# Performance work log

Hardware: AMD Instinct MI355X
Metric: run time of the kernel (lower is better)

The kernel has to match this reference:

```python
import jax, jax.numpy as jnp
import numpy as np

HEIGHT, WIDTH = 384, 640


def setup_inputs() -> dict:
    key = jax.random.key(0)
    ks = jax.random.split(key, 6)
    B, N, C_CLS, D = 8, 100, 92, 256
    return {
        "images": jax.random.normal(ks[0], (B, 3, HEIGHT, WIDTH), dtype=jnp.float32),
        "logits": jax.random.normal(ks[1], (B, N, C_CLS), dtype=jnp.float32),
        "pred_boxes": jax.random.uniform(ks[2], (B, N, 4), dtype=jnp.float32),
        "last_hidden_state": jax.random.normal(ks[3], (B, N, D), dtype=jnp.float32),
        "fc_w": jax.random.normal(ks[4], (256, D), dtype=jnp.float32) * 0.05,
        "fc_b": jax.random.normal(ks[5], (256,), dtype=jnp.float32) * 0.05,
    }


def reference(images, logits, pred_boxes, last_hidden_state, fc_w, fc_b):
    B = images.shape[0]
    num_objects = 2

    # probas computed in the original forward (unused in training mode -> DCE'd)
    probas = jax.nn.softmax(logits, axis=-1)[:, :, :-1]

    # cxcywh -> xyxy, scale by [W, H, W, H], truncate to int (torch .int())
    cx, cy, w, h = jnp.split(pred_boxes, 4, axis=-1)  # each [B, N, 1]
    xyxy = jnp.concatenate([cx - 0.5 * w, cy - 0.5 * h, cx + 0.5 * w, cy + 0.5 * h], axis=-1)
    img_dims = jnp.array([WIDTH, HEIGHT, WIDTH, HEIGHT], dtype=jnp.float32)
    bboxes = (xyxy * img_dims).astype(jnp.int32)  # [B, N, 4]

    # bboxes_to_mask (faithful to original, incl. its x/y axis convention):
    # x indexes rows (height), y indexes columns (width)
    x = jnp.arange(HEIGHT, dtype=jnp.float32)[:, None]   # [H, 1]
    y = jnp.arange(WIDTH, dtype=jnp.float32)[None, :]    # [1, W]
    bb = bboxes.astype(jnp.float32)[:, :, :, None, None]  # [B, N, 4, 1, 1]
    masks = (bb[:, :, 0] <= x) & (x <= bb[:, :, 2]) & (bb[:, :, 1] <= y) & (y <= bb[:, :, 3])  # [B, N, H, W]

    # diff images: sum channels, pairwise diff over (pre, post), abs, repeat x2 on batch
    summed = images.sum(axis=1).reshape(B // 2, 2, HEIGHT, WIDTH)
    diff = jnp.abs(summed[:, 1:] - summed[:, :1])          # [B/2, 1, H, W]
    diff = jnp.repeat(diff, 2, axis=0)                     # [B, 1, H, W]

    # masked mean score per box
    scores = jnp.mean(jnp.where(masks, diff, jnp.float32(0.0)), axis=(2, 3))  # [B, N]

    _, indices = jax.lax.top_k(scores, num_objects)        # [B, num_objects]
    h_i = jnp.take_along_axis(last_hidden_state, indices[:, :, None], axis=1)  # [B, O, D]
    h_i = h_i @ fc_w.T + fc_b                              # Linear: x W^T + b
    h_i = h_i.reshape(B // 2, 2, num_objects, -1)          # [b, i=2, O, hidden]
    return h_i[:, 0], h_i[:, 1]
```

## Files before the change

### kernel.cpp

```cpp
#include <hip/hip_runtime.h>

#define H_IMG 384
#define W_IMG 640
#define NPAIR 4
#define NBATCH 8
#define NBOX 100
#define DHID 256
#define ROWTILE 8
#define NTILES (H_IMG / ROWTILE)

__global__ __launch_bounds__(256) void k_sat_tile(const float* __restrict__ images,
                                                  float* __restrict__ sat,
                                                  float* __restrict__ totals_t) {
    __shared__ float buf[ROWTILE][W_IMG];

    const int p    = blockIdx.x / NTILES;
    const int tile = blockIdx.x % NTILES;
    const int lane = threadIdx.x & 63;
    const int wv   = threadIdx.x >> 6;
    const int r_lo = tile * ROWTILE;

    const size_t chw  = (size_t)H_IMG * W_IMG;
    const size_t chw2 = chw / 2;

    for (int rr = wv; rr < ROWTILE; rr += 4) {
        const int h = r_lo + rr;
        const float2* i0 = (const float2*)(images + ((size_t)(2 * p)     * 3 * H_IMG + h) * W_IMG);
        const float2* i1 = (const float2*)(images + ((size_t)(2 * p + 1) * 3 * H_IMG + h) * W_IMG);

        float dxv[5], dyv[5], s[5];
        #pragma unroll
        for (int k = 0; k < 5; ++k) {
            const int e = k * 64 + lane;
            float2 a0 = i0[e], b0 = i0[e + chw2], c0 = i0[e + 2 * chw2];
            float2 a1 = i1[e], b1 = i1[e + chw2], c1 = i1[e + 2 * chw2];
            dxv[k] = fabsf(((a1.x + b1.x) + c1.x) - ((a0.x + b0.x) + c0.x));
            dyv[k] = fabsf(((a1.y + b1.y) + c1.y) - ((a0.y + b0.y) + c0.y));
            s[k]   = dxv[k] + dyv[k];
        }

        #pragma unroll
        for (int off = 1; off < 64; off <<= 1) {
            float u0 = __shfl_up(s[0], off, 64);
            float u1 = __shfl_up(s[1], off, 64);
            float u2 = __shfl_up(s[2], off, 64);
            float u3 = __shfl_up(s[3], off, 64);
            float u4 = __shfl_up(s[4], off, 64);
            if (lane >= off) {
                s[0] += u0; s[1] += u1; s[2] += u2; s[3] += u3; s[4] += u4;
            }
        }

        const float t0 = __shfl(s[0], 63, 64);
        const float t1 = __shfl(s[1], 63, 64);
        const float t2 = __shfl(s[2], 63, 64);
        const float t3 = __shfl(s[3], 63, 64);
        float base[5];
        base[0] = 0.0f;
        base[1] = t0;
        base[2] = t0 + t1;
        base[3] = base[2] + t2;
        base[4] = base[3] + t3;

        float2* brow = (float2*)buf[rr];
        #pragma unroll
        for (int k = 0; k < 5; ++k) {
            const int e = k * 64 + lane;
            const float excl = base[k] + s[k] - (dxv[k] + dyv[k]);
            brow[e] = make_float2(excl + dxv[k], excl + dxv[k] + dyv[k]);
        }
    }
    __syncthreads();

    const int t = threadIdx.x;
    #pragma unroll
    for (int sub = 0; sub < 3; ++sub) {
        const int c = sub * 256 + t;
        if (c < W_IMG) {
            float run = 0.0f;
            float* gcol = sat + ((size_t)p * H_IMG + r_lo) * W_IMG + c;
            #pragma unroll
            for (int i = 0; i < ROWTILE; ++i) {
                run += buf[i][c];
                gcol[(size_t)i * W_IMG] = run;
            }
            totals_t[((size_t)p * W_IMG + c) * NTILES + tile] = run;
        }
    }
}

__global__ __launch_bounds__(256) void k_score_topk_fc(
        const float* __restrict__ sat,
        const float* __restrict__ totals_t,
        const float* __restrict__ pred_boxes,
        const float* __restrict__ lhs,
        const float* __restrict__ fc_w,
        const float* __restrict__ fc_b,
        float* __restrict__ out) {
    const int b = blockIdx.x;
    const int t = threadIdx.x;
    const int p = b >> 1;

    __shared__ float s_off[NTILES][W_IMG];
    __shared__ float s_score[NBOX];
    __shared__ int   s_idx[2];
    __shared__ float s_h[2][DHID];

    for (int c = t; c < W_IMG; c += 256) {
        const float4* tp = (const float4*)(totals_t + ((size_t)p * W_IMG + c) * NTILES);
        float run = 0.0f;
        #pragma unroll
        for (int q = 0; q < NTILES / 4; ++q) {
            const float4 v = tp[q];
            s_off[q * 4 + 0][c] = run; run += v.x;
            s_off[q * 4 + 1][c] = run; run += v.y;
            s_off[q * 4 + 2][c] = run; run += v.z;
            s_off[q * 4 + 3][c] = run; run += v.w;
        }
    }
    __syncthreads();

    const float* S = sat + (size_t)p * H_IMG * W_IMG;

    if (t < NBOX) {
        const float* pb = pred_boxes + ((size_t)b * NBOX + t) * 4;
        const float cx = pb[0], cy = pb[1], bw = pb[2], bh = pb[3];
        const int bb0 = (int)((cx - 0.5f * bw) * 640.0f);
        const int bb1 = (int)((cy - 0.5f * bh) * 384.0f);
        const int bb2 = (int)((cx + 0.5f * bw) * 640.0f);
        const int bb3 = (int)((cy + 0.5f * bh) * 384.0f);
        const int r0 = bb0 > 0 ? bb0 : 0;
        const int r2 = bb2 < H_IMG - 1 ? bb2 : H_IMG - 1;
        const int c0 = bb1 > 0 ? bb1 : 0;
        const int c2 = bb3 < W_IMG - 1 ? bb3 : W_IMG - 1;
        float sc = 0.0f;
        if (r0 <= r2 && c0 <= c2) {
            float sum = S[(size_t)r2 * W_IMG + c2] + s_off[r2 >> 3][c2];
            if (r0 > 0) sum -= S[(size_t)(r0 - 1) * W_IMG + c2] + s_off[(r0 - 1) >> 3][c2];
            if (c0 > 0) sum -= S[(size_t)r2 * W_IMG + (c0 - 1)] + s_off[r2 >> 3][c0 - 1];
            if (r0 > 0 && c0 > 0)
                sum += S[(size_t)(r0 - 1) * W_IMG + (c0 - 1)] + s_off[(r0 - 1) >> 3][c0 - 1];
            sc = sum / (float)(H_IMG * W_IMG);
        }
        s_score[t] = sc;
    }
    __syncthreads();

    if (t < 64) {
        float b0 = s_score[t];
        int   i0 = t;
        float b1 = -1e30f;
        int   i1 = 0x7fffffff;
        if (t + 64 < NBOX) {
            const float s1 = s_score[t + 64];
            if (s1 > b0) { b1 = b0; i1 = i0; b0 = s1; i0 = t + 64; }
            else         { b1 = s1; i1 = t + 64; }
        }
        #pragma unroll
        for (int off = 32; off > 0; off >>= 1) {
            const float o0 = __shfl_xor(b0, off, 64);
            const float o1 = __shfl_xor(b1, off, 64);
            const int   j0 = __shfl_xor(i0, off, 64);
            const int   j1 = __shfl_xor(i1, off, 64);
            const bool other_first = (o0 > b0) || (o0 == b0 && j0 < i0);
            if (other_first) {
                const bool mine2 = (b0 > o1) || (b0 == o1 && i0 < j1);
                const float n1 = mine2 ? b0 : o1;
                const int  nj1 = mine2 ? i0 : j1;
                b0 = o0; i0 = j0; b1 = n1; i1 = nj1;
            } else {
                const bool oth2 = (o0 > b1) || (o0 == b1 && j0 < i1);
                if (oth2) { b1 = o0; i1 = j0; }
            }
        }
        if (t == 0) { s_idx[0] = i0; s_idx[1] = i1; }
    }
    __syncthreads();

    s_h[0][t] = lhs[((size_t)b * NBOX + s_idx[0]) * DHID + t];
    s_h[1][t] = lhs[((size_t)b * NBOX + s_idx[1]) * DHID + t];
    __syncthreads();

    const float4* wrow4 = (const float4*)(fc_w + (size_t)t * DHID);
    float acc0 = fc_b[t];
    float acc1 = acc0;
    #pragma unroll 8
    for (int d4 = 0; d4 < DHID / 4; ++d4) {
        const float4 wv = wrow4[d4];
        const int d = d4 * 4;
        acc0 = fmaf(s_h[0][d + 0], wv.x, acc0);
        acc0 = fmaf(s_h[0][d + 1], wv.y, acc0);
        acc0 = fmaf(s_h[0][d + 2], wv.z, acc0);
        acc0 = fmaf(s_h[0][d + 3], wv.w, acc0);
        acc1 = fmaf(s_h[1][d + 0], wv.x, acc1);
        acc1 = fmaf(s_h[1][d + 1], wv.y, acc1);
        acc1 = fmaf(s_h[1][d + 2], wv.z, acc1);
        acc1 = fmaf(s_h[1][d + 3], wv.w, acc1);
    }

    const size_t base = (size_t)(b & 1) * (NPAIR * 2 * DHID) + (size_t)(b >> 1) * (2 * DHID);
    out[base + t]        = acc0;
    out[base + DHID + t] = acc1;
}

extern "C" void kernel_launch(void* const* d_in, const int* in_sizes, int n_in,
                              void* d_out, int out_size, void* d_ws, size_t ws_size,
                              hipStream_t stream) {
    const float* images     = (const float*)d_in[0];
    const float* pred_boxes = (const float*)d_in[2];
    const float* lhs        = (const float*)d_in[3];
    const float* fc_w       = (const float*)d_in[4];
    const float* fc_b       = (const float*)d_in[5];
    float* out              = (float*)d_out;

    float* sat      = (float*)d_ws;
    float* totals_t = sat + (size_t)NPAIR * H_IMG * W_IMG;

    hipLaunchKernelGGL(k_sat_tile, dim3(NPAIR * NTILES), dim3(256), 0, stream,
                       images, sat, totals_t);
    hipLaunchKernelGGL(k_score_topk_fc, dim3(NBATCH), dim3(256), 0, stream,
                       sat, totals_t, pred_boxes, lhs, fc_w, fc_b, out);
}
```

Measured before the change: 92.71 us.

## Compute per-tile box partial sums in-block instead of writing global SAT

The first kernel no longer writes the full summed-area table and column totals to global memory. Each 6-row tile block builds a local 2D prefix in shared memory and evaluates every box's contribution for that tile, writing per-tile partial sums. The second kernel reduces 64 partials per box before top-k and the FC. This removes the large SAT write and the random reads from it, in exchange for more per-block box work and a changed summation order. It also drops the division by H*W, which does not change the top-k ordering.

```diff
diff --git a/kernel.cpp b/kernel.cpp
--- a/kernel.cpp
+++ b/kernel.cpp
@@ -6,25 +6,25 @@
 #define NBATCH 8
 #define NBOX 100
 #define DHID 256
-#define ROWTILE 8
+#define ROWTILE 6
 #define NTILES (H_IMG / ROWTILE)
 
-__global__ __launch_bounds__(256) void k_sat_tile(const float* __restrict__ images,
-                                                  float* __restrict__ sat,
-                                                  float* __restrict__ totals_t) {
+__global__ __launch_bounds__(384) void k_tile_partial(const float* __restrict__ images,
+                                                      const float* __restrict__ pred_boxes,
+                                                      float* __restrict__ partial) {
     __shared__ float buf[ROWTILE][W_IMG];
 
-    const int p    = blockIdx.x / NTILES;
-    const int tile = blockIdx.x % NTILES;
-    const int lane = threadIdx.x & 63;
-    const int wv   = threadIdx.x >> 6;
+    const int p    = blockIdx.x >> 6;
+    const int tile = blockIdx.x & 63;
+    const int t    = threadIdx.x;
+    const int lane = t & 63;
+    const int wv   = t >> 6;
     const int r_lo = tile * ROWTILE;
 
-    const size_t chw  = (size_t)H_IMG * W_IMG;
-    const size_t chw2 = chw / 2;
-
-    for (int rr = wv; rr < ROWTILE; rr += 4) {
-        const int h = r_lo + rr;
+    const size_t chw2 = (size_t)H_IMG * W_IMG / 2;
+
+    {
+        const int h = r_lo + wv;
         const float2* i0 = (const float2*)(images + ((size_t)(2 * p)     * 3 * H_IMG + h) * W_IMG);
         const float2* i1 = (const float2*)(images + ((size_t)(2 * p + 1) * 3 * H_IMG + h) * W_IMG);
 
@@ -62,7 +62,7 @@
         base[3] = base[2] + t2;
         base[4] = base[3] + t3;
 
-        float2* brow = (float2*)buf[rr];
+        float2* brow = (float2*)buf[wv];
         #pragma unroll
         for (int k = 0; k < 5; ++k) {
             const int e = k * 64 + lane;
@@ -72,58 +72,18 @@
     }
     __syncthreads();
 
-    const int t = threadIdx.x;
-    #pragma unroll
-    for (int sub = 0; sub < 3; ++sub) {
-        const int c = sub * 256 + t;
-        if (c < W_IMG) {
-            float run = 0.0f;
-            float* gcol = sat + ((size_t)p * H_IMG + r_lo) * W_IMG + c;
-            #pragma unroll
-            for (int i = 0; i < ROWTILE; ++i) {
-                run += buf[i][c];
-                gcol[(size_t)i * W_IMG] = run;
-            }
-            totals_t[((size_t)p * W_IMG + c) * NTILES + tile] = run;
-        }
-    }
-}
-
-__global__ __launch_bounds__(256) void k_score_topk_fc(
-        const float* __restrict__ sat,
-        const float* __restrict__ totals_t,
-        const float* __restrict__ pred_boxes,
-        const float* __restrict__ lhs,
-        const float* __restrict__ fc_w,
-        const float* __restrict__ fc_b,
-        float* __restrict__ out) {
-    const int b = blockIdx.x;
-    const int t = threadIdx.x;
-    const int p = b >> 1;
-
-    __shared__ float s_off[NTILES][W_IMG];
-    __shared__ float s_score[NBOX];
-    __shared__ int   s_idx[2];
-    __shared__ float s_h[2][DHID];
-
-    for (int c = t; c < W_IMG; c += 256) {
-        const float4* tp = (const float4*)(totals_t + ((size_t)p * W_IMG + c) * NTILES);
+    for (int c = t; c < W_IMG; c += 384) {
         float run = 0.0f;
         #pragma unroll
-        for (int q = 0; q < NTILES / 4; ++q) {
-            const float4 v = tp[q];
-            s_off[q * 4 + 0][c] = run; run += v.x;
-            s_off[q * 4 + 1][c] = run; run += v.y;
-            s_off[q * 4 + 2][c] = run; run += v.z;
-            s_off[q * 4 + 3][c] = run; run += v.w;
-        }
-    }
-    __syncthreads();
-
-    const float* S = sat + (size_t)p * H_IMG * W_IMG;
-
-    if (t < NBOX) {
-        const float* pb = pred_boxes + ((size_t)b * NBOX + t) * 4;
+        for (int i = 0; i < ROWTILE; ++i) { run += buf[i][c]; buf[i][c] = run; }
+    }
+    __syncthreads();
+
+    if (t < 2 * NBOX) {
+        const int bb = t / NBOX;
+        const int n  = t - bb * NBOX;
+        const int b  = 2 * p + bb;
+        const float* pb = pred_boxes + ((size_t)b * NBOX + n) * 4;
         const float cx = pb[0], cy = pb[1], bw = pb[2], bh = pb[3];
         const int bb0 = (int)((cx - 0.5f * bw) * 640.0f);
         const int bb1 = (int)((cy - 0.5f * bh) * 384.0f);
@@ -133,16 +93,48 @@
         const int r2 = bb2 < H_IMG - 1 ? bb2 : H_IMG - 1;
         const int c0 = bb1 > 0 ? bb1 : 0;
         const int c2 = bb3 < W_IMG - 1 ? bb3 : W_IMG - 1;
+
+        const int a  = r0 > r_lo ? r0 : r_lo;
+        const int e  = r2 < r_lo + ROWTILE - 1 ? r2 : r_lo + ROWTILE - 1;
+
         float sc = 0.0f;
-        if (r0 <= r2 && c0 <= c2) {
-            float sum = S[(size_t)r2 * W_IMG + c2] + s_off[r2 >> 3][c2];
-            if (r0 > 0) sum -= S[(size_t)(r0 - 1) * W_IMG + c2] + s_off[(r0 - 1) >> 3][c2];
-            if (c0 > 0) sum -= S[(size_t)r2 * W_IMG + (c0 - 1)] + s_off[r2 >> 3][c0 - 1];
-            if (r0 > 0 && c0 > 0)
-                sum += S[(size_t)(r0 - 1) * W_IMG + (c0 - 1)] + s_off[(r0 - 1) >> 3][c0 - 1];
-            sc = sum / (float)(H_IMG * W_IMG);
-        }
-        s_score[t] = sc;
+        if (a <= e && c0 <= c2) {
+            const int ie = e - r_lo;
+            const int ia = a - r_lo - 1;
+            float sum = buf[ie][c2];
+            if (ia >= 0) sum -= buf[ia][c2];
+            if (c0 > 0) {
+                sum -= buf[ie][c0 - 1];
+                if (ia >= 0) sum += buf[ia][c0 - 1];
+            }
+            sc = sum;
+        }
+        partial[((size_t)b * NBOX + n) * NTILES + tile] = sc;
+    }
+}
+
+__global__ __launch_bounds__(256) void k_topk_fc(
+        const float* __restrict__ partial,
+        const float* __restrict__ lhs,
+        const float* __restrict__ fc_w,
+        const float* __restrict__ fc_b,
+        float* __restrict__ out) {
+    const int b = blockIdx.x;
+    const int t = threadIdx.x;
+
+    __shared__ float s_score[NBOX];
+    __shared__ int   s_idx[2];
+    __shared__ float s_h[2][DHID];
+
+    if (t < NBOX) {
+        const float4* pp = (const float4*)(partial + ((size_t)b * NBOX + t) * NTILES);
+        float a0 = 0.0f, a1 = 0.0f, a2 = 0.0f, a3 = 0.0f;
+        #pragma unroll
+        for (int q = 0; q < NTILES / 4; ++q) {
+            const float4 v = pp[q];
+            a0 += v.x; a1 += v.y; a2 += v.z; a3 += v.w;
+        }
+        s_score[t] = (a0 + a1) + (a2 + a3);
     }
     __syncthreads();
 
@@ -213,11 +205,10 @@
     const float* fc_b       = (const float*)d_in[5];
     float* out              = (float*)d_out;
 
-    float* sat      = (float*)d_ws;
-    float* totals_t = sat + (size_t)NPAIR * H_IMG * W_IMG;
-
-    hipLaunchKernelGGL(k_sat_tile, dim3(NPAIR * NTILES), dim3(256), 0, stream,
-                       images, sat, totals_t);
-    hipLaunchKernelGGL(k_score_topk_fc, dim3(NBATCH), dim3(256), 0, stream,
-                       sat, totals_t, pred_boxes, lhs, fc_w, fc_b, out);
+    float* partial = (float*)d_ws;
+
+    hipLaunchKernelGGL(k_tile_partial, dim3(NPAIR * NTILES), dim3(384), 0, stream,
+                       images, pred_boxes, partial);
+    hipLaunchKernelGGL(k_topk_fc, dim3(NBATCH), dim3(256), 0, stream,
+                       partial, lhs, fc_w, fc_b, out);
 }
```

New measurement: 88.60 us. 4.4% less time.
